# Kernel tuning notes

Hardware: AMD Instinct MI355X
Metric: run time of the kernel (lower is better)

Reference implementation:

```python
import jax, jax.numpy as jnp
import numpy as np

BS, T, N, E = 4, 6, 400, 3000
D = 100        # object_dim == state_dim == out_fts (forced by code)
NS = 30        # num states
NOBJ = 300     # object vocab
NET = 10       # n edge types
NSTEPS = 3     # GatedGraphConv n_steps


def setup_inputs() -> dict:
    key = jax.random.key(0)
    ks = jax.random.split(key, 16)
    def nrm(k, shape, s=0.05):
        return jax.random.normal(k, shape, jnp.float32) * s
    return dict(
        class_names=jax.random.randint(ks[0], (BS, T, N), 0, NOBJ),
        states=jax.random.uniform(ks[1], (BS, T, N, NS), jnp.float32),
        edges=jax.random.randint(ks[2], (BS, T, E, 2), 0, N),
        edge_types=jax.random.randint(ks[3], (BS, T, E), 0, NET),
        visibility=jax.random.uniform(ks[4], (BS, T, N), jnp.float32),
        mask_edges=jnp.ones((BS, T, E), jnp.float32),
        obj_emb=nrm(ks[5], (NOBJ, D)),
        state_W=nrm(ks[6], (D, NS)), state_b=jnp.zeros((D,), jnp.float32),
        c1_W=nrm(ks[7], (D, 2 * D)), c1_b=jnp.zeros((D,), jnp.float32),
        c2_W=nrm(ks[8], (D, D)), c2_b=jnp.zeros((D,), jnp.float32),
        edge_embed=nrm(ks[9], (NET, D * D)),
        g_wih=nrm(ks[10], (3 * D, D)), g_whh=nrm(ks[11], (3 * D, D)),
        g_bih=jnp.zeros((3 * D,), jnp.float32), g_bhh=jnp.zeros((3 * D,), jnp.float32),
        o_wih=nrm(ks[12], (3 * D, D)), o_whh=nrm(ks[13], (3 * D, D)),
    )


def _gru(x, h, wih, whh, bih=None, bhh=None):
    # torch.nn.GRUCell semantics
    gi = x @ wih.T
    gh = h @ whh.T
    if bih is not None:
        gi = gi + bih
        gh = gh + bhh
    ir, iz, inn = jnp.split(gi, 3, axis=-1)
    hr, hz, hn = jnp.split(gh, 3, axis=-1)
    r = jax.nn.sigmoid(ir + hr)
    z = jax.nn.sigmoid(iz + hz)
    n = jnp.tanh(inn + r * hn)
    return (1.0 - z) * n + z * h


def reference(class_names, states, edges, edge_types, visibility, mask_edges,
              obj_emb, state_W, state_b, c1_W, c1_b, c2_W, c2_b,
              edge_embed, g_wih, g_whh, g_bih, g_bhh, o_wih, o_whh):
    bs, t_len, n = class_names.shape
    # initial node representation (ClassNameStateRepresentation)
    emb = obj_emb[class_names]                       # [bs,T,N,D]
    st = states @ state_W.T + state_b                # [bs,T,N,D]
    x = jnp.concatenate([emb, st], -1)
    x = jax.nn.relu(x @ c1_W.T + c1_b) @ c2_W.T + c2_b  # [bs,T,N,D]

    off = (jnp.arange(bs) * n)[:, None]              # flatten batch into node axis
    h = jnp.zeros((bs * n, D), x.dtype)              # outer temporal GRU state
    reprs = []
    for t in range(t_len):
        h = _gru(x[:, t].reshape(bs * n, D), h, o_wih, o_whh)  # bias=False
        feat_flat = h                                 # [bs*N, D]
        src = (edges[:, t, :, 0] + off).reshape(-1)   # [bs*E]
        dst = (edges[:, t, :, 1] + off).reshape(-1)
        # per-edge DxD matrices, masked (as in original)
        W = edge_embed[edge_types[:, t].reshape(-1)].reshape(-1, D, D)
        W = W * mask_edges[:, t].reshape(-1)[:, None, None]
        # NOTE: original never updates feat_flat inside the n_steps loop,
        # so every step reads the same source features; we replicate that.
        feat_out = feat_flat
        for _ in range(NSTEPS):
            msg = jnp.einsum('eij,ej->ei', W, feat_flat[src])           # per-edge matvec
            a = jax.ops.segment_sum(msg, dst, num_segments=bs * n)     # scatter-add
            feat_out = _gru(a, feat_flat, g_wih, g_whh, g_bih, g_bhh)
        reprs.append(feat_out.reshape(bs, n, D) * visibility[:, t, :, None])
    node_reprs = jnp.stack(reprs, 1)                  # [bs,T,N,D]
    num_nodes = visibility.sum(-1) + 1e-9             # [bs,T]
    global_repr = (node_reprs * visibility[..., None]).sum(2) / num_nodes[..., None]
    return node_reprs, global_repr
```

## Files before the change

kernel.cpp:

```cpp
#include <hip/hip_runtime.h>

#define BSZ   4
#define TT    6
#define NNODE 400
#define EED   3000
#define DDIM  100
#define NSDIM 30
#define NETYP 10
#define BN    (BSZ*NNODE)
#define NROW  (BSZ*TT*NNODE)
#define NEDGE (BSZ*TT*EED)
#define KPAD  1024

#define OFF_PRE1 0
#define OFF_QT   30000
#define OFF_BQ   33000
#define OFF_BF   33104
#define OFF_WIT  33408
#define OFF_BI   63408
#define OFF_BH   63744
#define OFF_WFH  64080
#define OFF_WFL  85584
#define OFF_WOH  107088
#define OFF_WOL  128592
#define OFF_BWF  150096
#define OFF_BWPK 450096
#define OFF_WHPK 622128
#define OFF_HALL 643632
#define OFF_START 1603632
#define OFF_SE   1613236
#define OFF_INV  1685248
#define OFF_GI   1685280

typedef __attribute__((ext_vector_type(8))) short bf16x8;
typedef __attribute__((ext_vector_type(4))) float f32x4;

__device__ __forceinline__ float sigf(float v) { return 1.0f / (1.0f + expf(-v)); }

__device__ __forceinline__ short bfc(float f) {
    union { float f; unsigned u; } v; v.f = f;
    unsigned r = v.u + 0x7fffu + ((v.u >> 16) & 1u);
    return (short)(r >> 16);
}

__device__ __forceinline__ float bf2f(short h) {
    union { unsigned u; float f; } x; x.u = ((unsigned)(unsigned short)h) << 16;
    return x.f;
}

__device__ __forceinline__ unsigned cvtpk(float lo, float hi) {
    unsigned r;
    asm("v_cvt_pk_bf16_f32 %0, %1, %2" : "=v"(r) : "v"(lo), "v"(hi));
    return r;
}

__global__ __launch_bounds__(256) void k_front(
    const float* __restrict__ obj_emb, const float* __restrict__ c1_W,
    const float* __restrict__ c1_b, const float* __restrict__ state_W,
    const float* __restrict__ state_b, const float* __restrict__ c2_W,
    const float* __restrict__ c2_b, const float* __restrict__ o_wih,
    const float* __restrict__ o_whh, const float* __restrict__ g_wih,
    const float* __restrict__ g_bih, const float* __restrict__ g_bhh,
    const float* __restrict__ vis, const int* __restrict__ edges,
    float* __restrict__ pre1, float* __restrict__ QT, float* __restrict__ bQ,
    float* __restrict__ bfold, float* __restrict__ WiT,
    float* __restrict__ bI, float* __restrict__ bH,
    ushort* __restrict__ WFH, ushort* __restrict__ WFL,
    ushort* __restrict__ WOH, ushort* __restrict__ WOL,
    float* __restrict__ inv_nv, float* __restrict__ gout,
    int* __restrict__ start, int* __restrict__ sortedE) {
    int tid = threadIdx.x;
    if (blockIdx.x < 24) {
        __shared__ int hcnt[400];
        __shared__ int hstart[400];
        int c = blockIdx.x;
        int t = c >> 2, b = c & 3;
        int febase = (b * TT + t) * EED;
        for (int i = tid; i < 400; i += 256) hcnt[i] = 0;
        __syncthreads();
        for (int i = tid; i < EED; i += 256)
            atomicAdd(&hcnt[edges[(febase + i) * 2 + 1]], 1);
        __syncthreads();
        if (tid < 64) {
            int lane = tid, carry = 0;
            for (int ch = 0; ch < 7; ++ch) {
                int idx = ch * 64 + lane;
                int orig = (idx < 400) ? hcnt[idx] : 0;
                int v = orig;
                #pragma unroll
                for (int off = 1; off < 64; off <<= 1) {
                    int u = __shfl_up(v, off, 64);
                    if (lane >= off) v += u;
                }
                if (idx < 400) hstart[idx] = carry + (v - orig);
                carry += __shfl(v, 63, 64);
            }
        }
        __syncthreads();
        for (int i = tid; i < 400; i += 256) {
            start[c * 400 + i] = c * EED + hstart[i];
            hcnt[i] = hstart[i];
        }
        if (c == 23 && tid == 0) start[NROW] = NEDGE;
        __syncthreads();
        for (int i = tid; i < EED; i += 256) {
            int fe = febase + i;
            int dst = edges[fe * 2 + 1];
            int pos = atomicAdd(&hcnt[dst], 1);
            sortedE[c * EED + pos] = fe;
        }
        return;
    }
    int i = (blockIdx.x - 24) * 256 + tid;
    if (i < 30000) {
        int cls = i / DDIM, d1 = i % DDIM;
        float acc = 0.f;
        for (int k = 0; k < DDIM; ++k)
            acc += obj_emb[cls * DDIM + k] * c1_W[d1 * 2 * DDIM + k];
        pre1[i] = acc;
    } else if (i < 33000) {
        int j = i - 30000, s = j / DDIM, d1 = j % DDIM;
        float acc = 0.f;
        for (int d = 0; d < DDIM; ++d)
            acc += c1_W[d1 * 2 * DDIM + DDIM + d] * state_W[d * NSDIM + s];
        QT[j] = acc;
    } else if (i < 33100) {
        int d1 = i - 33000;
        float acc = c1_b[d1];
        for (int d = 0; d < DDIM; ++d)
            acc += state_b[d] * c1_W[d1 * 2 * DDIM + DDIM + d];
        bQ[d1] = acc;
    } else if (i < 33400) {
        int o = i - 33100;
        float acc = 0.f;
        for (int d = 0; d < DDIM; ++d)
            acc += o_wih[o * DDIM + d] * c2_b[d];
        bfold[o] = acc;
    } else if (i < 76408) {
        int e = i - 33400;
        int j = e & 7, frag = e >> 3;
        int l = frag & 63, ct = (frag >> 6) % 21, kt = frag / (21 * 64);
        int col = ct * 16 + (l & 15);
        int gate = col / 112, dd = col % 112;
        int k = kt * 32 + ((l >> 4) << 3) + j;
        float v = 0.f;
        if (k < DDIM && dd < DDIM) {
            int o = gate * DDIM + dd;
            for (int d = 0; d < DDIM; ++d)
                v += o_wih[o * DDIM + d] * c2_W[d * DDIM + k];
        }
        short hi = bfc(v);
        WFH[frag * 8 + j] = (ushort)hi;
        WFL[frag * 8 + j] = (ushort)bfc(v - bf2f(hi));
    } else if (i < 119416) {
        int e = i - 76408;
        int j = e & 7, frag = e >> 3;
        int l = frag & 63, ct = (frag >> 6) % 21, kt = frag / (21 * 64);
        int col = ct * 16 + (l & 15);
        int gate = col / 112, dd = col % 112;
        int k = kt * 32 + ((l >> 4) << 3) + j;
        float v = 0.f;
        if (k < DDIM && dd < DDIM)
            v = o_whh[(gate * DDIM + dd) * DDIM + k];
        short hi = bfc(v);
        WOH[frag * 8 + j] = (ushort)hi;
        WOL[frag * 8 + j] = (ushort)bfc(v - bf2f(hi));
    } else if (i < 149416) {
        int j = i - 119416, k = j / 300, o = j % 300;
        WiT[j] = g_wih[o * DDIM + k];
    } else if (i < 149752) {
        int col = i - 149416, gate = col / 112, o = col % 112;
        bI[col] = (o < DDIM) ? g_bih[gate * DDIM + o] : 0.f;
    } else if (i < 150088) {
        int col = i - 149752, gate = col / 112, o = col % 112;
        bH[col] = (o < DDIM) ? g_bhh[gate * DDIM + o] : 0.f;
    } else if (i >= 150144 && i < 151680) {
        int g = (i - 150144) >> 6;
        int lane = i & 63;
        float s = 0.f;
        for (int n = lane; n < NNODE; n += 64)
            s += vis[g * NNODE + n];
        #pragma unroll
        for (int off = 32; off > 0; off >>= 1)
            s += __shfl_down(s, off, 64);
        if (lane == 0) inv_nv[g] = 1.f / (s + 1e-9f);
    } else if (i >= 151680 && i < 154080) {
        gout[i - 151680] = 0.f;
    }
}

__global__ __launch_bounds__(448) void k_mid(
    const float* __restrict__ edge_embed, const float* __restrict__ WiT,
    float* __restrict__ BW,
    const int* __restrict__ cls, const float* __restrict__ states,
    const float* __restrict__ pre1, const float* __restrict__ QT,
    const float* __restrict__ bQ, const float* __restrict__ bfold,
    const bf16x8* __restrict__ WFH, const bf16x8* __restrict__ WFL,
    float* __restrict__ GI) {
    __shared__ float st_lds[16 * NSDIM];
    __shared__ float hid_lds[16 * 112];
    __shared__ int cls_lds[16];
    int tid = threadIdx.x;
    if (blockIdx.x < 670) {
        int i = blockIdx.x * 448 + tid;
        if (i < 1000 * 300) {
            int kk = i / 300, go = i % 300;
            int g = kk / DDIM, k = kk % DDIM;
            const float* es = edge_embed + g * DDIM * DDIM + k;
            float acc = 0.f;
            for (int j = 0; j < DDIM; ++j)
                acc += es[j * DDIM] * WiT[j * 300 + go];
            BW[i] = acc;
        }
        return;
    }
    int r0 = (blockIdx.x - 670) * 16;
    for (int idx = tid; idx < 16 * NSDIM; idx += 448) st_lds[idx] = states[r0 * NSDIM + idx];
    if (tid < 16) cls_lds[tid] = cls[r0 + tid];
    __syncthreads();
    #pragma unroll
    for (int u = 0; u < 4; ++u) {
        int it = tid + u * 448;
        if (it < 1600) {
            int n = it / 100, d = it % 100;
            float acc = bQ[d] + pre1[cls_lds[n] * DDIM + d];
            for (int s = 0; s < NSDIM; ++s)
                acc += QT[s * DDIM + d] * st_lds[n * NSDIM + s];
            hid_lds[n * 112 + d] = fmaxf(acc, 0.f);
        }
    }
    __syncthreads();
    int w = tid >> 6, l = tid & 63, rit = l & 15, kgrp = l >> 4;
    f32x4 acc3[3];
    acc3[0] = acc3[1] = acc3[2] = (f32x4){0.f, 0.f, 0.f, 0.f};
    for (int kt = 0; kt < 4; ++kt) {
        bf16x8 Ahi, Alo;
        #pragma unroll
        for (int j = 0; j < 8; ++j) {
            int k = kt * 32 + kgrp * 8 + j;
            float v = (k < DDIM) ? hid_lds[rit * 112 + k] : 0.f;
            short hi = bfc(v);
            Ahi[j] = hi;
            Alo[j] = bfc(v - bf2f(hi));
        }
        #pragma unroll
        for (int p = 0; p < 3; ++p) {
            int ct = w + p * 7;
            bf16x8 Bhi = WFH[(kt * 21 + ct) * 64 + l];
            bf16x8 Blo = WFL[(kt * 21 + ct) * 64 + l];
            acc3[p] = __builtin_amdgcn_mfma_f32_16x16x32_bf16(Ahi, Bhi, acc3[p], 0, 0, 0);
            acc3[p] = __builtin_amdgcn_mfma_f32_16x16x32_bf16(Alo, Bhi, acc3[p], 0, 0, 0);
            acc3[p] = __builtin_amdgcn_mfma_f32_16x16x32_bf16(Ahi, Blo, acc3[p], 0, 0, 0);
        }
    }
    int dd = w * 16 + rit;
    if (dd < DDIM) {
        int b = r0 / (TT * NNODE), t = (r0 / NNODE) % TT, nn0 = r0 % NNODE;
        int trow0 = t * BN + b * NNODE + nn0;
        #pragma unroll
        for (int p = 0; p < 3; ++p) {
            float bias = bfold[p * DDIM + dd];
            #pragma unroll
            for (int j = 0; j < 4; ++j) {
                int row = kgrp * 4 + j;
                GI[(trow0 + row) * 336 + p * 112 + dd] = acc3[p][j] + bias;
            }
        }
    }
}

__global__ __launch_bounds__(448) void k_mid2(const float* __restrict__ GI,
    const bf16x8* __restrict__ WOH, const bf16x8* __restrict__ WOL,
    float* __restrict__ Hall,
    const float* __restrict__ BW, const float* __restrict__ g_whh,
    bf16x8* __restrict__ BWpk, bf16x8* __restrict__ WHpk) {
    __shared__ float h_lds[16 * 112];
    int tid = threadIdx.x;
    if (blockIdx.x >= 100) {
        int i = (blockIdx.x - 100) * 448 + tid;
        if (i < 43008) {
            int l = i & 63, c = (i >> 6) % 21, kt = i / (21 * 64);
            int col = c * 16 + (l & 15);
            int gate = col / 112, o = col % 112;
            bf16x8 r;
            #pragma unroll
            for (int j = 0; j < 8; ++j) {
                int kk = kt * 32 + ((l >> 4) << 3) + j;
                float v = (kk < 1000 && o < DDIM) ? BW[kk * 300 + gate * DDIM + o] : 0.f;
                r[j] = bfc(v);
            }
            BWpk[i] = r;
        } else if (i < 48384) {
            int id = i - 43008;
            int l = id & 63, c = (id >> 6) % 21, kt2 = id / (21 * 64);
            int col = c * 16 + (l & 15);
            int gate = col / 112, o = col % 112;
            bf16x8 r;
            #pragma unroll
            for (int j = 0; j < 8; ++j) {
                int k = kt2 * 32 + ((l >> 4) << 3) + j;
                float v = (k < DDIM && o < DDIM) ? g_whh[(gate * DDIM + o) * DDIM + k] : 0.f;
                r[j] = bfc(v);
            }
            WHpk[id] = r;
        }
        return;
    }
    int bn0 = blockIdx.x * 16;
    for (int idx = tid; idx < 16 * 112; idx += 448) h_lds[idx] = 0.f;
    __syncthreads();
    int w = tid >> 6, l = tid & 63, rit = l & 15, kgrp = l >> 4;
    int dd = w * 16 + rit;
    for (int t = 0; t < TT; ++t) {
        float gir[4], giz[4], gin[4], hold[4];
        if (dd < DDIM) {
            #pragma unroll
            for (int j = 0; j < 4; ++j) {
                int node = kgrp * 4 + j;
                int trow = t * BN + bn0 + node;
                gir[j] = GI[trow * 336 + dd];
                giz[j] = GI[trow * 336 + 112 + dd];
                gin[j] = GI[trow * 336 + 224 + dd];
                hold[j] = h_lds[node * 112 + dd];
            }
        }
        f32x4 a0 = (f32x4){0.f, 0.f, 0.f, 0.f};
        f32x4 a1 = (f32x4){0.f, 0.f, 0.f, 0.f};
        f32x4 a2 = (f32x4){0.f, 0.f, 0.f, 0.f};
        if (t > 0) {
            for (int kt = 0; kt < 4; ++kt) {
                bf16x8 Ahi, Alo;
                #pragma unroll
                for (int j = 0; j < 8; ++j) {
                    int k = kt * 32 + kgrp * 8 + j;
                    float v = (k < DDIM) ? h_lds[rit * 112 + k] : 0.f;
                    short hi = bfc(v);
                    Ahi[j] = hi;
                    Alo[j] = bfc(v - bf2f(hi));
                }
                {
                    bf16x8 Bhi = WOH[(kt * 21 + w) * 64 + l];
                    bf16x8 Blo = WOL[(kt * 21 + w) * 64 + l];
                    a0 = __builtin_amdgcn_mfma_f32_16x16x32_bf16(Ahi, Bhi, a0, 0, 0, 0);
                    a0 = __builtin_amdgcn_mfma_f32_16x16x32_bf16(Alo, Bhi, a0, 0, 0, 0);
                    a0 = __builtin_amdgcn_mfma_f32_16x16x32_bf16(Ahi, Blo, a0, 0, 0, 0);
                }
                {
                    bf16x8 Bhi = WOH[(kt * 21 + w + 7) * 64 + l];
                    bf16x8 Blo = WOL[(kt * 21 + w + 7) * 64 + l];
                    a1 = __builtin_amdgcn_mfma_f32_16x16x32_bf16(Ahi, Bhi, a1, 0, 0, 0);
                    a1 = __builtin_amdgcn_mfma_f32_16x16x32_bf16(Alo, Bhi, a1, 0, 0, 0);
                    a1 = __builtin_amdgcn_mfma_f32_16x16x32_bf16(Ahi, Blo, a1, 0, 0, 0);
                }
                {
                    bf16x8 Bhi = WOH[(kt * 21 + w + 14) * 64 + l];
                    bf16x8 Blo = WOL[(kt * 21 + w + 14) * 64 + l];
                    a2 = __builtin_amdgcn_mfma_f32_16x16x32_bf16(Ahi, Bhi, a2, 0, 0, 0);
                    a2 = __builtin_amdgcn_mfma_f32_16x16x32_bf16(Alo, Bhi, a2, 0, 0, 0);
                    a2 = __builtin_amdgcn_mfma_f32_16x16x32_bf16(Ahi, Blo, a2, 0, 0, 0);
                }
            }
        }
        __syncthreads();
        if (dd < DDIM) {
            #pragma unroll
            for (int j = 0; j < 4; ++j) {
                int node = kgrp * 4 + j;
                int trow = t * BN + bn0 + node;
                float r = sigf(gir[j] + a0[j]);
                float z = sigf(giz[j] + a1[j]);
                float nn = tanhf(gin[j] + r * a2[j]);
                float hnew = (1.f - z) * nn + z * hold[j];
                h_lds[node * 112 + dd] = hnew;
                Hall[trow * DDIM + dd] = hnew;
            }
        }
        __syncthreads();
    }
}

template<int G>
__device__ __forceinline__ void gacc2(float* acc, const float* __restrict__ hs,
                                      float m, int l) {
    constexpr int k0 = 100 * G, k1 = k0 + 100;
    constexpr int J0 = k0 >> 7, J1 = (k1 - 1) >> 7;
    #pragma unroll
    for (int j = J0; j <= J1; ++j) {
        int s = 128 * j + 2 * l;
        if (s >= k0 && s < k1) {
            float2 hv = *(const float2*)(hs + (s - k0));
            acc[2 * j]     += m * hv.x;
            acc[2 * j + 1] += m * hv.y;
        }
    }
}

__global__ __launch_bounds__(448) void k_fused32(
    const int* __restrict__ edges, const int* __restrict__ etype,
    const float* __restrict__ emask, const int* __restrict__ start,
    const int* __restrict__ sortedE,
    const bf16x8* __restrict__ BWpk, const bf16x8* __restrict__ WHpk,
    const float* __restrict__ bI, const float* __restrict__ bH,
    const float* __restrict__ Hall, const float* __restrict__ visv,
    const float* __restrict__ inv_nv, float* __restrict__ out,
    float* __restrict__ gout) {
    __shared__ unsigned lds[16384];
    int tid = threadIdx.x;
    int w = tid >> 6, l = tid & 63;
    int rit = l & 15, kgrp = l >> 4;
    int rbase = blockIdx.x * 32;

    for (int r = w; r < 32; r += 7) {
        int trd = rbase + r;
        int s0 = start[trd], s1 = start[trd + 1];
        int rowbase = (trd / NNODE) * NNODE;
        float acc[16];
        #pragma unroll
        for (int j = 0; j < 16; ++j) acc[j] = 0.f;
        for (int e = s0; e < s1; ++e) {
            int fe = sortedE[e];
            float m = emask[fe];
            int src = edges[fe * 2 + 0];
            int g = etype[fe];
            const float* hs = Hall + (size_t)(rowbase + src) * DDIM;
            switch (g) {
                case 0: gacc2<0>(acc, hs, m, l); break;
                case 1: gacc2<1>(acc, hs, m, l); break;
                case 2: gacc2<2>(acc, hs, m, l); break;
                case 3: gacc2<3>(acc, hs, m, l); break;
                case 4: gacc2<4>(acc, hs, m, l); break;
                case 5: gacc2<5>(acc, hs, m, l); break;
                case 6: gacc2<6>(acc, hs, m, l); break;
                case 7: gacc2<7>(acc, hs, m, l); break;
                case 8: gacc2<8>(acc, hs, m, l); break;
                case 9: gacc2<9>(acc, hs, m, l); break;
            }
        }
        #pragma unroll
        for (int j = 0; j < 8; ++j) {
            unsigned word = cvtpk(acc[2 * j], acc[2 * j + 1]);
            int g16 = 16 * j + (l >> 2);
            int wd = r * 512 + ((g16 * 4) ^ ((r & 7) << 2)) + (l & 3);
            lds[wd] = word;
        }
    }
    __syncthreads();

    f32x4 acc[2][3];
    #pragma unroll
    for (int mt = 0; mt < 2; ++mt)
        #pragma unroll
        for (int q = 0; q < 3; ++q) acc[mt][q] = (f32x4){0.f, 0.f, 0.f, 0.f};

    for (int kt = 0; kt < 32; ++kt) {
        bf16x8 fb0 = BWpk[(kt * 21 + w) * 64 + l];
        bf16x8 fb1 = BWpk[(kt * 21 + w + 7) * 64 + l];
        bf16x8 fb2 = BWpk[(kt * 21 + w + 14) * 64 + l];
        #pragma unroll
        for (int mt = 0; mt < 2; ++mt) {
            int row = mt * 16 + rit;
            int wd = row * 512 + (((kt * 16 + kgrp * 4)) ^ ((row & 7) << 2));
            bf16x8 fa = *(bf16x8*)&lds[wd];
            acc[mt][0] = __builtin_amdgcn_mfma_f32_16x16x32_bf16(fa, fb0, acc[mt][0], 0, 0, 0);
            acc[mt][1] = __builtin_amdgcn_mfma_f32_16x16x32_bf16(fa, fb1, acc[mt][1], 0, 0, 0);
            acc[mt][2] = __builtin_amdgcn_mfma_f32_16x16x32_bf16(fa, fb2, acc[mt][2], 0, 0, 0);
        }
    }
    __syncthreads();

    for (int i = tid; i < 512; i += 448) {
        int row = i >> 4, g16 = i & 15;
        int k0 = g16 * 8;
        const float* hs = Hall + (size_t)(rbase + row) * DDIM;
        float v[8];
        #pragma unroll
        for (int jj = 0; jj < 8; ++jj)
            v[jj] = (k0 + jj < DDIM) ? hs[k0 + jj] : 0.f;
        int4 wv;
        wv.x = (int)cvtpk(v[0], v[1]);
        wv.y = (int)cvtpk(v[2], v[3]);
        wv.z = (int)cvtpk(v[4], v[5]);
        wv.w = (int)cvtpk(v[6], v[7]);
        int wd = row * 64 + ((g16 * 4) ^ ((row & 7) << 2));
        *(int4*)&lds[wd] = wv;
    }
    __syncthreads();

    f32x4 hacc[2];
    hacc[0] = (f32x4){0.f, 0.f, 0.f, 0.f};
    hacc[1] = (f32x4){0.f, 0.f, 0.f, 0.f};
    for (int kt2 = 0; kt2 < 4; ++kt2) {
        bf16x8 fb0 = WHpk[(kt2 * 21 + w) * 64 + l];
        bf16x8 fb1 = WHpk[(kt2 * 21 + w + 7) * 64 + l];
        bf16x8 fb2 = WHpk[(kt2 * 21 + w + 14) * 64 + l];
        #pragma unroll
        for (int mt = 0; mt < 2; ++mt) {
            int row = mt * 16 + rit;
            int wd = row * 64 + (((kt2 * 16 + kgrp * 4)) ^ ((row & 7) << 2));
            bf16x8 fh = *(bf16x8*)&lds[wd];
            acc[mt][0] = __builtin_amdgcn_mfma_f32_16x16x32_bf16(fh, fb0, acc[mt][0], 0, 0, 0);
            acc[mt][1] = __builtin_amdgcn_mfma_f32_16x16x32_bf16(fh, fb1, acc[mt][1], 0, 0, 0);
            hacc[mt]  = __builtin_amdgcn_mfma_f32_16x16x32_bf16(fh, fb2, hacc[mt], 0, 0, 0);
        }
    }

    int col = w * 16 + rit;
    if (col < DDIM) {
        float bIr = bI[col], bIz = bI[112 + col], bIn = bI[224 + col];
        float bHr = bH[col], bHz = bH[112 + col], bHn = bH[224 + col];
        int t = rbase / BN;
        #pragma unroll
        for (int mt = 0; mt < 2; ++mt) {
            int r2 = (rbase + mt * 16) % BN;
            int b = r2 / NNODE, n0 = r2 % NNODE;
            int bt = b * TT + t;
            int trow0 = rbase + mt * 16 + kgrp * 4;
            int brow0 = bt * NNODE + n0 + kgrp * 4;
            float gs = 0.f;
            #pragma unroll
            for (int j = 0; j < 4; ++j) {
                float r = sigf(acc[mt][0][j] + bIr + bHr);
                float z = sigf(acc[mt][1][j] + bIz + bHz);
                float ghn = hacc[mt][j] + bHn;
                float nn = tanhf(acc[mt][2][j] + bIn + r * ghn);
                float hold = Hall[(trow0 + j) * DDIM + col];
                float feat = (1.f - z) * nn + z * hold;
                int brow = brow0 + j;
                float v = visv[brow];
                float outv = feat * v;
                out[brow * DDIM + col] = outv;
                gs += outv * v;
            }
            gs += __shfl_xor(gs, 16, 64);
            gs += __shfl_xor(gs, 32, 64);
            if (kgrp == 0)
                atomicAdd(&gout[bt * DDIM + col], gs * inv_nv[bt]);
        }
    }
}

extern "C" void kernel_launch(void* const* d_in, const int* in_sizes, int n_in,
                              void* d_out, int out_size, void* d_ws, size_t ws_size,
                              hipStream_t stream) {
    const int*   class_names = (const int*)d_in[0];
    const float* states      = (const float*)d_in[1];
    const int*   edges       = (const int*)d_in[2];
    const int*   edge_types  = (const int*)d_in[3];
    const float* visibility  = (const float*)d_in[4];
    const float* mask_edges  = (const float*)d_in[5];
    const float* obj_emb     = (const float*)d_in[6];
    const float* state_W     = (const float*)d_in[7];
    const float* state_b     = (const float*)d_in[8];
    const float* c1_W        = (const float*)d_in[9];
    const float* c1_b        = (const float*)d_in[10];
    const float* c2_W        = (const float*)d_in[11];
    const float* c2_b        = (const float*)d_in[12];
    const float* edge_embed  = (const float*)d_in[13];
    const float* g_wih       = (const float*)d_in[14];
    const float* g_whh       = (const float*)d_in[15];
    const float* g_bih       = (const float*)d_in[16];
    const float* g_bhh       = (const float*)d_in[17];
    const float* o_wih       = (const float*)d_in[18];
    const float* o_whh       = (const float*)d_in[19];

    float* out = (float*)d_out;
    float* gout = out + (size_t)NROW * DDIM;
    float* ws  = (float*)d_ws;
    float*  pre1  = ws + OFF_PRE1;
    float*  QT    = ws + OFF_QT;
    float*  bQ    = ws + OFF_BQ;
    float*  bfold = ws + OFF_BF;
    float*  WiT   = ws + OFF_WIT;
    float*  bI    = ws + OFF_BI;
    float*  bH    = ws + OFF_BH;
    ushort* WFH   = (ushort*)(ws + OFF_WFH);
    ushort* WFL   = (ushort*)(ws + OFF_WFL);
    ushort* WOH   = (ushort*)(ws + OFF_WOH);
    ushort* WOL   = (ushort*)(ws + OFF_WOL);
    float*  BWf   = ws + OFF_BWF;
    bf16x8* BWpk  = (bf16x8*)(ws + OFF_BWPK);
    bf16x8* WHpk  = (bf16x8*)(ws + OFF_WHPK);
    float*  Hall  = ws + OFF_HALL;
    int*    start = (int*)(ws + OFF_START);
    int*    sortedE = (int*)(ws + OFF_SE);
    float*  inv_nv= ws + OFF_INV;
    float*  GI    = ws + OFF_GI;

    k_front<<<626, 256, 0, stream>>>(obj_emb, c1_W, c1_b, state_W, state_b,
                                     c2_W, c2_b, o_wih, o_whh, g_wih, g_bih, g_bhh,
                                     visibility, edges, pre1, QT, bQ, bfold, WiT,
                                     bI, bH, WFH, WFL, WOH, WOL, inv_nv, gout,
                                     start, sortedE);
    k_mid<<<1270, 448, 0, stream>>>(edge_embed, WiT, BWf, class_names, states,
                                    pre1, QT, bQ, bfold,
                                    (const bf16x8*)WFH, (const bf16x8*)WFL, GI);
    k_mid2<<<208, 448, 0, stream>>>(GI, (const bf16x8*)WOH, (const bf16x8*)WOL,
                                    Hall, BWf, g_whh, BWpk, WHpk);
    k_fused32<<<NROW / 32, 448, 0, stream>>>(edges, edge_types, mask_edges,
                                             start, sortedE, BWpk, WHpk, bI, bH,
                                             Hall, visibility, inv_nv, out, gout);
}
```

Baseline: 128.0 us.

## Pack edge records at sort time, batch edge gathers, halve fused-kernel row tile

When sorting edges, the front kernel now packs source index, edge type and mask into one int2 record, so the aggregation loop reads a single record instead of three dependent gathers. The per-edge gather loop is unrolled by four, issuing all Hall loads before accumulating, which adds memory-level parallelism. The fused GRU kernel tile drops from 32 to 16 rows per block, doubling the grid and halving LDS use to raise occupancy. The cost is that the B operand weights are reloaded twice as often per row and the workspace layout is enlarged.

```diff
diff --git a/kernel.cpp b/kernel.cpp
--- a/kernel.cpp
+++ b/kernel.cpp
@@ -29,8 +29,8 @@
 #define OFF_HALL 643632
 #define OFF_START 1603632
 #define OFF_SE   1613236
-#define OFF_INV  1685248
-#define OFF_GI   1685280
+#define OFF_INV  1757248
+#define OFF_GI   1757280
 
 typedef __attribute__((ext_vector_type(8))) short bf16x8;
 typedef __attribute__((ext_vector_type(4))) float f32x4;
@@ -62,13 +62,14 @@
     const float* __restrict__ o_whh, const float* __restrict__ g_wih,
     const float* __restrict__ g_bih, const float* __restrict__ g_bhh,
     const float* __restrict__ vis, const int* __restrict__ edges,
+    const int* __restrict__ etype, const float* __restrict__ emask,
     float* __restrict__ pre1, float* __restrict__ QT, float* __restrict__ bQ,
     float* __restrict__ bfold, float* __restrict__ WiT,
     float* __restrict__ bI, float* __restrict__ bH,
     ushort* __restrict__ WFH, ushort* __restrict__ WFL,
     ushort* __restrict__ WOH, ushort* __restrict__ WOL,
     float* __restrict__ inv_nv, float* __restrict__ gout,
-    int* __restrict__ start, int* __restrict__ sortedE) {
+    int* __restrict__ start, int2* __restrict__ sortedE2) {
     int tid = threadIdx.x;
     if (blockIdx.x < 24) {
         __shared__ int hcnt[400];
@@ -105,9 +106,11 @@
         __syncthreads();
         for (int i = tid; i < EED; i += 256) {
             int fe = febase + i;
-            int dst = edges[fe * 2 + 1];
-            int pos = atomicAdd(&hcnt[dst], 1);
-            sortedE[c * EED + pos] = fe;
+            int2 ed = *(const int2*)(edges + fe * 2);
+            int pos = atomicAdd(&hcnt[ed.y], 1);
+            int g = etype[fe];
+            float m = emask[fe];
+            sortedE2[c * EED + pos] = make_int2(ed.x | (g << 16), __float_as_int(m));
         }
         return;
     }
@@ -379,61 +382,64 @@
     }
 }
 
-template<int G>
-__device__ __forceinline__ void gacc2(float* acc, const float* __restrict__ hs,
-                                      float m, int l) {
-    constexpr int k0 = 100 * G, k1 = k0 + 100;
-    constexpr int J0 = k0 >> 7, J1 = (k1 - 1) >> 7;
-    #pragma unroll
-    for (int j = J0; j <= J1; ++j) {
-        int s = 128 * j + 2 * l;
-        if (s >= k0 && s < k1) {
-            float2 hv = *(const float2*)(hs + (s - k0));
-            acc[2 * j]     += m * hv.x;
-            acc[2 * j + 1] += m * hv.y;
-        }
-    }
-}
-
-__global__ __launch_bounds__(448) void k_fused32(
-    const int* __restrict__ edges, const int* __restrict__ etype,
-    const float* __restrict__ emask, const int* __restrict__ start,
-    const int* __restrict__ sortedE,
+__global__ __launch_bounds__(448) void k_fused16(
+    const int* __restrict__ start, const int2* __restrict__ sortedE2,
     const bf16x8* __restrict__ BWpk, const bf16x8* __restrict__ WHpk,
     const float* __restrict__ bI, const float* __restrict__ bH,
     const float* __restrict__ Hall, const float* __restrict__ visv,
     const float* __restrict__ inv_nv, float* __restrict__ out,
     float* __restrict__ gout) {
-    __shared__ unsigned lds[16384];
+    __shared__ unsigned lds[8192];
     int tid = threadIdx.x;
     int w = tid >> 6, l = tid & 63;
     int rit = l & 15, kgrp = l >> 4;
-    int rbase = blockIdx.x * 32;
-
-    for (int r = w; r < 32; r += 7) {
+    int rbase = blockIdx.x * 16;
+
+    for (int r = w; r < 16; r += 7) {
         int trd = rbase + r;
         int s0 = start[trd], s1 = start[trd + 1];
         int rowbase = (trd / NNODE) * NNODE;
         float acc[16];
         #pragma unroll
         for (int j = 0; j < 16; ++j) acc[j] = 0.f;
-        for (int e = s0; e < s1; ++e) {
-            int fe = sortedE[e];
-            float m = emask[fe];
-            int src = edges[fe * 2 + 0];
-            int g = etype[fe];
-            const float* hs = Hall + (size_t)(rowbase + src) * DDIM;
-            switch (g) {
-                case 0: gacc2<0>(acc, hs, m, l); break;
-                case 1: gacc2<1>(acc, hs, m, l); break;
-                case 2: gacc2<2>(acc, hs, m, l); break;
-                case 3: gacc2<3>(acc, hs, m, l); break;
-                case 4: gacc2<4>(acc, hs, m, l); break;
-                case 5: gacc2<5>(acc, hs, m, l); break;
-                case 6: gacc2<6>(acc, hs, m, l); break;
-                case 7: gacc2<7>(acc, hs, m, l); break;
-                case 8: gacc2<8>(acc, hs, m, l); break;
-                case 9: gacc2<9>(acc, hs, m, l); break;
+        for (int e0 = s0; e0 < s1; e0 += 4) {
+            float2 hA[4], hB[4];
+            float me[4];
+            int ge[4];
+            #pragma unroll
+            for (int e = 0; e < 4; ++e) {
+                int idx = e0 + e;
+                int2 rec = (idx < s1) ? sortedE2[idx] : make_int2(0, 0);
+                int src = rec.x & 0xffff;
+                int g = rec.x >> 16;
+                ge[e] = g;
+                me[e] = __int_as_float(rec.y);
+                const float* hs = Hall + (size_t)(rowbase + src) * DDIM;
+                int k0 = g * 100;
+                int J0 = k0 >> 7, J1 = (k0 + 99) >> 7;
+                int sA = 128 * J0 + 2 * l, sB = 128 * J1 + 2 * l;
+                bool aA = (sA >= k0) && (sA < k0 + 100);
+                bool aB = (J1 != J0) && (sB >= k0) && (sB < k0 + 100);
+                hA[e] = aA ? *(const float2*)(hs + (sA - k0)) : make_float2(0.f, 0.f);
+                hB[e] = aB ? *(const float2*)(hs + (sB - k0)) : make_float2(0.f, 0.f);
+            }
+            #pragma unroll
+            for (int e = 0; e < 4; ++e) {
+                float m = me[e];
+                float ax = m * hA[e].x, ay = m * hA[e].y;
+                float bx = m * hB[e].x, by = m * hB[e].y;
+                switch (ge[e]) {
+                    case 0: acc[0] += ax; acc[1] += ay; break;
+                    case 1: acc[0] += ax; acc[1] += ay; acc[2] += bx; acc[3] += by; break;
+                    case 2: acc[2] += ax; acc[3] += ay; acc[4] += bx; acc[5] += by; break;
+                    case 3: acc[4] += ax; acc[5] += ay; acc[6] += bx; acc[7] += by; break;
+                    case 4: acc[6] += ax; acc[7] += ay; break;
+                    case 5: acc[6] += ax; acc[7] += ay; acc[8] += bx; acc[9] += by; break;
+                    case 6: acc[8] += ax; acc[9] += ay; acc[10] += bx; acc[11] += by; break;
+                    case 7: acc[10] += ax; acc[11] += ay; acc[12] += bx; acc[13] += by; break;
+                    case 8: acc[12] += ax; acc[13] += ay; acc[14] += bx; acc[15] += by; break;
+                    case 9: acc[14] += ax; acc[15] += ay; break;
+                }
             }
         }
         #pragma unroll
@@ -446,29 +452,22 @@
     }
     __syncthreads();
 
-    f32x4 acc[2][3];
-    #pragma unroll
-    for (int mt = 0; mt < 2; ++mt)
-        #pragma unroll
-        for (int q = 0; q < 3; ++q) acc[mt][q] = (f32x4){0.f, 0.f, 0.f, 0.f};
+    f32x4 acc[3];
+    acc[0] = acc[1] = acc[2] = (f32x4){0.f, 0.f, 0.f, 0.f};
 
     for (int kt = 0; kt < 32; ++kt) {
         bf16x8 fb0 = BWpk[(kt * 21 + w) * 64 + l];
         bf16x8 fb1 = BWpk[(kt * 21 + w + 7) * 64 + l];
         bf16x8 fb2 = BWpk[(kt * 21 + w + 14) * 64 + l];
-        #pragma unroll
-        for (int mt = 0; mt < 2; ++mt) {
-            int row = mt * 16 + rit;
-            int wd = row * 512 + (((kt * 16 + kgrp * 4)) ^ ((row & 7) << 2));
-            bf16x8 fa = *(bf16x8*)&lds[wd];
-            acc[mt][0] = __builtin_amdgcn_mfma_f32_16x16x32_bf16(fa, fb0, acc[mt][0], 0, 0, 0);
-            acc[mt][1] = __builtin_amdgcn_mfma_f32_16x16x32_bf16(fa, fb1, acc[mt][1], 0, 0, 0);
-            acc[mt][2] = __builtin_amdgcn_mfma_f32_16x16x32_bf16(fa, fb2, acc[mt][2], 0, 0, 0);
-        }
+        int wd = rit * 512 + (((kt * 16 + kgrp * 4)) ^ ((rit & 7) << 2));
+        bf16x8 fa = *(bf16x8*)&lds[wd];
+        acc[0] = __builtin_amdgcn_mfma_f32_16x16x32_bf16(fa, fb0, acc[0], 0, 0, 0);
+        acc[1] = __builtin_amdgcn_mfma_f32_16x16x32_bf16(fa, fb1, acc[1], 0, 0, 0);
+        acc[2] = __builtin_amdgcn_mfma_f32_16x16x32_bf16(fa, fb2, acc[2], 0, 0, 0);
     }
     __syncthreads();
 
-    for (int i = tid; i < 512; i += 448) {
+    for (int i = tid; i < 256; i += 448) {
         int row = i >> 4, g16 = i & 15;
         int k0 = g16 * 8;
         const float* hs = Hall + (size_t)(rbase + row) * DDIM;
@@ -486,56 +485,45 @@
     }
     __syncthreads();
 
-    f32x4 hacc[2];
-    hacc[0] = (f32x4){0.f, 0.f, 0.f, 0.f};
-    hacc[1] = (f32x4){0.f, 0.f, 0.f, 0.f};
+    f32x4 hacc = (f32x4){0.f, 0.f, 0.f, 0.f};
     for (int kt2 = 0; kt2 < 4; ++kt2) {
         bf16x8 fb0 = WHpk[(kt2 * 21 + w) * 64 + l];
         bf16x8 fb1 = WHpk[(kt2 * 21 + w + 7) * 64 + l];
         bf16x8 fb2 = WHpk[(kt2 * 21 + w + 14) * 64 + l];
-        #pragma unroll
-        for (int mt = 0; mt < 2; ++mt) {
-            int row = mt * 16 + rit;
-            int wd = row * 64 + (((kt2 * 16 + kgrp * 4)) ^ ((row & 7) << 2));
-            bf16x8 fh = *(bf16x8*)&lds[wd];
-            acc[mt][0] = __builtin_amdgcn_mfma_f32_16x16x32_bf16(fh, fb0, acc[mt][0], 0, 0, 0);
-            acc[mt][1] = __builtin_amdgcn_mfma_f32_16x16x32_bf16(fh, fb1, acc[mt][1], 0, 0, 0);
-            hacc[mt]  = __builtin_amdgcn_mfma_f32_16x16x32_bf16(fh, fb2, hacc[mt], 0, 0, 0);
-        }
+        int wd = rit * 64 + (((kt2 * 16 + kgrp * 4)) ^ ((rit & 7) << 2));
+        bf16x8 fh = *(bf16x8*)&lds[wd];
+        acc[0] = __builtin_amdgcn_mfma_f32_16x16x32_bf16(fh, fb0, acc[0], 0, 0, 0);
+        acc[1] = __builtin_amdgcn_mfma_f32_16x16x32_bf16(fh, fb1, acc[1], 0, 0, 0);
+        hacc   = __builtin_amdgcn_mfma_f32_16x16x32_bf16(fh, fb2, hacc, 0, 0, 0);
     }
 
     int col = w * 16 + rit;
     if (col < DDIM) {
         float bIr = bI[col], bIz = bI[112 + col], bIn = bI[224 + col];
         float bHr = bH[col], bHz = bH[112 + col], bHn = bH[224 + col];
-        int t = rbase / BN;
-        #pragma unroll
-        for (int mt = 0; mt < 2; ++mt) {
-            int r2 = (rbase + mt * 16) % BN;
-            int b = r2 / NNODE, n0 = r2 % NNODE;
-            int bt = b * TT + t;
-            int trow0 = rbase + mt * 16 + kgrp * 4;
-            int brow0 = bt * NNODE + n0 + kgrp * 4;
-            float gs = 0.f;
-            #pragma unroll
-            for (int j = 0; j < 4; ++j) {
-                float r = sigf(acc[mt][0][j] + bIr + bHr);
-                float z = sigf(acc[mt][1][j] + bIz + bHz);
-                float ghn = hacc[mt][j] + bHn;
-                float nn = tanhf(acc[mt][2][j] + bIn + r * ghn);
-                float hold = Hall[(trow0 + j) * DDIM + col];
-                float feat = (1.f - z) * nn + z * hold;
-                int brow = brow0 + j;
-                float v = visv[brow];
-                float outv = feat * v;
-                out[brow * DDIM + col] = outv;
-                gs += outv * v;
-            }
-            gs += __shfl_xor(gs, 16, 64);
-            gs += __shfl_xor(gs, 32, 64);
-            if (kgrp == 0)
-                atomicAdd(&gout[bt * DDIM + col], gs * inv_nv[bt]);
-        }
+        int t = rbase / BN, r2 = rbase % BN, b = r2 / NNODE, n0 = r2 % NNODE;
+        int bt = b * TT + t;
+        int trow0 = rbase + kgrp * 4;
+        int brow0 = bt * NNODE + n0 + kgrp * 4;
+        float gs = 0.f;
+        #pragma unroll
+        for (int j = 0; j < 4; ++j) {
+            float r = sigf(acc[0][j] + bIr + bHr);
+            float z = sigf(acc[1][j] + bIz + bHz);
+            float ghn = hacc[j] + bHn;
+            float nn = tanhf(acc[2][j] + bIn + r * ghn);
+            float hold = Hall[(trow0 + j) * DDIM + col];
+            float feat = (1.f - z) * nn + z * hold;
+            int brow = brow0 + j;
+            float v = visv[brow];
+            float outv = feat * v;
+            out[brow * DDIM + col] = outv;
+            gs += outv * v;
+        }
+        gs += __shfl_xor(gs, 16, 64);
+        gs += __shfl_xor(gs, 32, 64);
+        if (kgrp == 0)
+            atomicAdd(&gout[bt * DDIM + col], gs * inv_nv[bt]);
     }
 }
 
@@ -582,21 +570,21 @@
     bf16x8* WHpk  = (bf16x8*)(ws + OFF_WHPK);
     float*  Hall  = ws + OFF_HALL;
     int*    start = (int*)(ws + OFF_START);
-    int*    sortedE = (int*)(ws + OFF_SE);
+    int2*   sortedE2 = (int2*)(ws + OFF_SE);
     float*  inv_nv= ws + OFF_INV;
     float*  GI    = ws + OFF_GI;
 
     k_front<<<626, 256, 0, stream>>>(obj_emb, c1_W, c1_b, state_W, state_b,
                                      c2_W, c2_b, o_wih, o_whh, g_wih, g_bih, g_bhh,
-                                     visibility, edges, pre1, QT, bQ, bfold, WiT,
-                                     bI, bH, WFH, WFL, WOH, WOL, inv_nv, gout,
-                                     start, sortedE);
+                                     visibility, edges, edge_types, mask_edges,
+                                     pre1, QT, bQ, bfold, WiT, bI, bH,
+                                     WFH, WFL, WOH, WOL, inv_nv, gout,
+                                     start, sortedE2);
     k_mid<<<1270, 448, 0, stream>>>(edge_embed, WiT, BWf, class_names, states,
                                     pre1, QT, bQ, bfold,
                                     (const bf16x8*)WFH, (const bf16x8*)WFL, GI);
     k_mid2<<<208, 448, 0, stream>>>(GI, (const bf16x8*)WOH, (const bf16x8*)WOL,
                                     Hall, BWf, g_whh, BWpk, WHpk);
-    k_fused32<<<NROW / 32, 448, 0, stream>>>(edges, edge_types, mask_edges,
-                                             start, sortedE, BWpk, WHpk, bI, bH,
+    k_fused16<<<NROW / 16, 448, 0, stream>>>(start, sortedE2, BWpk, WHpk, bI, bH,
                                              Hall, visibility, inv_nv, out, gout);
 }
```

New measurement: 118.1 us. 1.08x faster.
